# Kernel tuning notes

Measured on AMD Instinct MI355X. Metric: run time of the kernel, lower is better.

The kernel has to match this reference:

```python
import jax, jax.numpy as jnp
import numpy as np

B, N, DIM, NL, E = 8, 4096, 128, 3, 524288
NN = B * N


def setup_inputs() -> dict:
    key = jax.random.key(0)
    kx, ke, kw = jax.random.split(key, 3)
    x = jax.random.normal(kx, (B, N, DIM), dtype=jnp.float32)
    batch_edge_index = jax.random.randint(ke, (2, E), 0, NN, dtype=jnp.int32)
    wks = jax.random.split(kw, NL)
    Ws = jnp.stack([jax.random.normal(k, (DIM, DIM), dtype=jnp.float32) / np.sqrt(DIM)
                    for k in wks])  # [NL, DIM, DIM]
    bs = jnp.zeros((NL, DIM), dtype=jnp.float32)
    return {"x": x, "batch_edge_index": batch_edge_index, "Ws": Ws, "bs": bs}


def _gcn_layer(x, W, b, row, col, deg_inv_sqrt, n):
    # PyG GCNConv: h = x @ W; symmetric normalization over edges+self-loops;
    # scatter-add messages at targets (col); add bias.
    h = x @ W  # [n, DIM]
    norm = deg_inv_sqrt[row] * deg_inv_sqrt[col]  # [E+n]
    msg = h[row] * norm[:, None]  # gather at sources, scale
    return jax.ops.segment_sum(msg, col, num_segments=n) + b


def reference(x, batch_edge_index, Ws, bs):
    nb, npts, d = x.shape
    n = nb * npts
    h = x.reshape(n, d)
    # add self-loops once (same edge structure for all layers)
    loops = jnp.arange(n, dtype=batch_edge_index.dtype)
    row = jnp.concatenate([batch_edge_index[0], loops])
    col = jnp.concatenate([batch_edge_index[1], loops])
    deg = jax.ops.segment_sum(jnp.ones_like(col, dtype=h.dtype), col, num_segments=n)
    deg_inv_sqrt = jnp.where(deg > 0, jax.lax.rsqrt(jnp.maximum(deg, 1e-12)), 0.0)
    for i in range(NL):
        out = _gcn_layer(h, Ws[i], bs[i], row, col, deg_inv_sqrt, n)
        h = jax.nn.relu(h + out)  # residual + relu (dropout = identity in eval)
    return h.reshape(nb, npts, d)
```

## Files before the change

kernel.cpp:

```cpp
#include <hip/hip_runtime.h>


typedef __attribute__((ext_vector_type(8))) short short8;
typedef __attribute__((ext_vector_type(4))) float f32x4;
typedef __attribute__((ext_vector_type(2))) float f32x2;
typedef __attribute__((ext_vector_type(2))) unsigned u32x2;

__device__ inline ushort f2bf(float f) {
    union { float f; unsigned u; } v; v.f = f;
    unsigned u = v.u;
    return (ushort)((u + 0x7fffu + ((u >> 16) & 1u)) >> 16);
}
__device__ inline float2 bf2f(unsigned u) {
    union { unsigned i; float f; } a, b;
    a.i = u << 16;
    b.i = u & 0xffff0000u;
    return make_float2(a.f, b.f);
}
__device__ inline f32x4 bf4(u32x2 v) {
    float2 a = bf2f(v.x), b = bf2f(v.y);
    f32x4 r = { a.x, a.y, b.x, b.y };
    return r;
}
__device__ inline short8 pack8(f32x4 a, f32x4 b) {
    short8 r = { (short)f2bf(a.x), (short)f2bf(a.y), (short)f2bf(a.z), (short)f2bf(a.w),
                 (short)f2bf(b.x), (short)f2bf(b.y), (short)f2bf(b.z), (short)f2bf(b.w) };
    return r;
}
__device__ inline unsigned char f2fp8(float f) {
    return (unsigned char)(__builtin_amdgcn_cvt_pk_fp8_f32(f, f, 0, false) & 0xff);
}
__device__ inline f32x4 fp8x4(unsigned v) {
    f32x2 lo = __builtin_amdgcn_cvt_pk_f32_fp8((int)v, false);
    f32x2 hi = __builtin_amdgcn_cvt_pk_f32_fp8((int)v, true);
    f32x4 r = { lo.x, lo.y, hi.x, hi.y };
    return r;
}

__global__ void k_zero(int* __restrict__ p, int m) {
    int i = blockIdx.x * blockDim.x + threadIdx.x;
    if (i < m) p[i] = 0;
}

__global__ void k_deg(const int* __restrict__ col, int* __restrict__ deg, int E) {
    int i = blockIdx.x * blockDim.x + threadIdx.x;
    if (i < E) atomicAdd(&deg[col[i]], 1);
}

__global__ __launch_bounds__(256) void k_scan1(const int* __restrict__ deg,
                                               int* __restrict__ offs,
                                               int* __restrict__ bsum, int n) {
    __shared__ int sm[256];
    int t = threadIdx.x, i = blockIdx.x * 256 + t;
    int v = (i < n) ? deg[i] : 0;
    sm[t] = v;
    __syncthreads();
    for (int off = 1; off < 256; off <<= 1) {
        int u = (t >= off) ? sm[t - off] : 0;
        __syncthreads();
        sm[t] += u;
        __syncthreads();
    }
    if (i < n) offs[i] = sm[t] - v;
    if (t == 255) bsum[blockIdx.x] = sm[255];
}

__global__ __launch_bounds__(256) void k_scan3(int* __restrict__ offs,
                                               const int* __restrict__ bsum,
                                               const int* __restrict__ deg,
                                               int* __restrict__ cnt,
                                               float* __restrict__ dis,
                                               unsigned* __restrict__ g32,
                                               int n, int E) {
    __shared__ int red[256];
    int t = threadIdx.x, bid = blockIdx.x;
    red[t] = (t < 128 && t < bid) ? bsum[t] : 0;
    __syncthreads();
    for (int off = 128; off >= 1; off >>= 1) {
        if (t < off) red[t] += red[t + off];
        __syncthreads();
    }
    int base = red[0];
    int i = bid * 256 + t;
    if (i < n) {
        int o = offs[i] + base;
        offs[i] = o;
        cnt[i] = o;
        dis[i] = rsqrtf((float)(deg[i] + 1));
    }
    if (i == 0) offs[n] = E;
    if (i < 32) g32[(size_t)n * 32 + i] = 0;
}

#define GEMM_MAIN(A0, A1, A2, A3)                                               \
    f32x4 acc[8] = {};                                                          \
    _Pragma("unroll")                                                           \
    for (int nf = 0; nf < 8; ++nf) {                                            \
        const unsigned* wr = &Wl[nf * 16 + c][0];                               \
        int sx = (c & 7) << 2;                                                  \
        int b = q * 4;                                                          \
        short8 b0 = *(const short8*)(wr + ((b +  0) ^ sx));                     \
        short8 b1 = *(const short8*)(wr + ((b + 16) ^ sx));                     \
        short8 b2 = *(const short8*)(wr + ((b + 32) ^ sx));                     \
        short8 b3 = *(const short8*)(wr + ((b + 48) ^ sx));                     \
        acc[nf] = __builtin_amdgcn_mfma_f32_16x16x32_bf16(A0, b0, acc[nf], 0, 0, 0); \
        acc[nf] = __builtin_amdgcn_mfma_f32_16x16x32_bf16(A1, b1, acc[nf], 0, 0, 0); \
        acc[nf] = __builtin_amdgcn_mfma_f32_16x16x32_bf16(A2, b2, acc[nf], 0, 0, 0); \
        acc[nf] = __builtin_amdgcn_mfma_f32_16x16x32_bf16(A3, b3, acc[nf], 0, 0, 0); \
    }

#define GEMM_STORE(D0, D1, D2, D3)                                              \
    _Pragma("unroll")                                                           \
    for (int nf = 0; nf < 8; ++nf) {                                            \
        int gc = nf * 16 + c;                                                   \
        g[(size_t)(rb + q * 4 + 0) * 128 + gc] = f2fp8(acc[nf][0] * (D0));      \
        g[(size_t)(rb + q * 4 + 1) * 128 + gc] = f2fp8(acc[nf][1] * (D1));      \
        g[(size_t)(rb + q * 4 + 2) * 128 + gc] = f2fp8(acc[nf][2] * (D2));      \
        g[(size_t)(rb + q * 4 + 3) * 128 + gc] = f2fp8(acc[nf][3] * (D3));      \
    }

#define W_STAGE(TILE)                                                            \
    __shared__ unsigned Wl[128][64];                                             \
    int tid = threadIdx.x;                                                       \
    {                                                                            \
        int nn = tid & 127, hf = tid >> 7;                                       \
        for (int qq = 0; qq < 32; ++qq) {                                        \
            int k2 = hf * 32 + qq;                                               \
            float lo = W[(size_t)(2 * k2) * 128 + nn];                           \
            float hi = W[(size_t)(2 * k2 + 1) * 128 + nn];                       \
            Wl[nn][k2 ^ ((nn & 7) << 2)] = ((unsigned)f2bf(hi) << 16) | f2bf(lo);\
        }                                                                        \
    }                                                                            \
    __syncthreads();                                                             \
    int w = tid >> 6, l = tid & 63;                                              \
    int rb = (TILE) * 64 + w * 16;                                               \
    int c = l & 15, q = l >> 4;

__global__ __launch_bounds__(256) void k_gemm(const unsigned* __restrict__ hb,
                                              const float* __restrict__ W,
                                              const float* __restrict__ dis,
                                              unsigned char* __restrict__ g, int n) {
    W_STAGE(blockIdx.x)
    const short8* arow = (const short8*)(hb + (size_t)(rb + c) * 64);
    short8 a0 = __builtin_nontemporal_load(&arow[q]);
    short8 a1 = __builtin_nontemporal_load(&arow[4 + q]);
    short8 a2 = __builtin_nontemporal_load(&arow[8 + q]);
    short8 a3 = __builtin_nontemporal_load(&arow[12 + q]);
    GEMM_MAIN(a0, a1, a2, a3)
    float d0 = dis[rb + q * 4 + 0], d1 = dis[rb + q * 4 + 1];
    float d2 = dis[rb + q * 4 + 2], d3 = dis[rb + q * 4 + 3];
    GEMM_STORE(d0, d1, d2, d3)
}

__global__ __launch_bounds__(256) void k_l0b(const float* __restrict__ x,
                                             const float* __restrict__ W,
                                             const float* __restrict__ dis,
                                             unsigned char* __restrict__ g,
                                             const int* __restrict__ rowp,
                                             const int* __restrict__ colp,
                                             int* __restrict__ cnt,
                                             ushort* __restrict__ csru,
                                             int n, int E) {
    int gtiles = n >> 6;
    if ((int)blockIdx.x >= gtiles) {
        int i = ((int)blockIdx.x - gtiles) * 256 + threadIdx.x;
        if (i < E) {
            int cc = colp[i];
            int p = atomicAdd(&cnt[cc], 1);
            csru[p] = (ushort)rowp[i];
        }
        return;
    }
    W_STAGE((int)blockIdx.x)
    const f32x4* xr = (const f32x4*)(x + (size_t)(rb + c) * 128);
    short8 a0 = pack8(xr[q * 2 +  0], xr[q * 2 +  1]);
    short8 a1 = pack8(xr[q * 2 +  8], xr[q * 2 +  9]);
    short8 a2 = pack8(xr[q * 2 + 16], xr[q * 2 + 17]);
    short8 a3 = pack8(xr[q * 2 + 24], xr[q * 2 + 25]);
    GEMM_MAIN(a0, a1, a2, a3)
    float d0 = dis[rb + q * 4 + 0], d1 = dis[rb + q * 4 + 1];
    float d2 = dis[rb + q * 4 + 2], d3 = dis[rb + q * 4 + 3];
    GEMM_STORE(d0, d1, d2, d3)
}

__global__ __launch_bounds__(256) void k_gather(const unsigned* __restrict__ g32,
                                                unsigned* __restrict__ hb,
                                                const float* __restrict__ dis,
                                                const float* __restrict__ bias,
                                                const int* __restrict__ offs,
                                                const ushort* __restrict__ csru,
                                                const float* __restrict__ xres,
                                                float* __restrict__ outp,
                                                int n, int use_x, int last) {
    int wid = threadIdx.x >> 6, lane = threadIdx.x & 63;
    int sel = lane >> 5, hl = lane & 31;
    int node = blockIdx.x * 8 + wid * 2 + sel;
    if (node >= n) return;

    float dn = dis[node];
    f32x4 bv = ((const f32x4*)bias)[hl];
    f32x4 hv;
    if (use_x) {
        hv = __builtin_nontemporal_load(&((const f32x4*)xres)[(size_t)node * 32 + hl]);
    } else {
        u32x2 h2 = __builtin_nontemporal_load(&((const u32x2*)hb)[(size_t)node * 32 + hl]);
        hv = bf4(h2);
    }

    f32x4 acc = fp8x4(g32[(size_t)node * 32 + hl]);
    int s = offs[node];
    int deg = offs[node + 1] - s;
    for (int j0 = 0; j0 < deg; j0 += 32) {
        int rem = deg - j0;
        int m = rem < 32 ? rem : 32;
        int idx = (hl < m) ? (int)__builtin_nontemporal_load(&csru[s + j0 + hl]) : n;
        int mc = (m + 7) & ~7;
        unsigned v[32];
#pragma unroll
        for (int b = 0; b < 4; ++b) {
            if (b * 8 < mc) {
#pragma unroll
                for (int u = 0; u < 8; ++u) {
                    int r = __shfl(idx, b * 8 + u, 32);
                    v[b * 8 + u] = g32[(size_t)r * 32 + hl];
                }
            }
        }
#pragma unroll
        for (int b = 0; b < 4; ++b) {
            if (b * 8 < mc) {
                f32x4 s0 = (fp8x4(v[b * 8 + 0]) + fp8x4(v[b * 8 + 1])) +
                           (fp8x4(v[b * 8 + 2]) + fp8x4(v[b * 8 + 3]));
                f32x4 s1 = (fp8x4(v[b * 8 + 4]) + fp8x4(v[b * 8 + 5])) +
                           (fp8x4(v[b * 8 + 6]) + fp8x4(v[b * 8 + 7]));
                acc += s0 + s1;
            }
        }
    }

    f32x4 o = acc * dn + hv + bv;
    o.x = fmaxf(o.x, 0.f); o.y = fmaxf(o.y, 0.f);
    o.z = fmaxf(o.z, 0.f); o.w = fmaxf(o.w, 0.f);
    if (last) {
        __builtin_nontemporal_store(o, &((f32x4*)outp)[(size_t)node * 32 + hl]);
    } else {
        u32x2 pk;
        pk.x = ((unsigned)f2bf(o.y) << 16) | f2bf(o.x);
        pk.y = ((unsigned)f2bf(o.w) << 16) | f2bf(o.z);
        __builtin_nontemporal_store(pk, &((u32x2*)hb)[(size_t)node * 32 + hl]);
    }
}

static inline size_t al256(size_t x) { return (x + 255) & ~(size_t)255; }

extern "C" void kernel_launch(void* const* d_in, const int* in_sizes, int n_in,
                              void* d_out, int out_size, void* d_ws, size_t ws_size,
                              hipStream_t stream) {
    const float* x  = (const float*)d_in[0];
    const int*   ei = (const int*)d_in[1];
    const float* Ws = (const float*)d_in[2];
    const float* bs = (const float*)d_in[3];
    int n  = in_sizes[0] / 128;
    int E  = in_sizes[1] / 2;
    int NL = in_sizes[2] / (128 * 128);
    const int* rowp = ei;
    const int* colp = ei + E;

    char* ws = (char*)d_ws;
    size_t gplane  = al256((size_t)(n + 1) * 128);
    size_t hplane  = al256((size_t)(n + 1) * 256);
    unsigned char* g  = (unsigned char*)ws;
    unsigned*      hb = (unsigned*)(ws + gplane);
    char* p = ws + gplane + hplane;
    float* dis  = (float*)p;               p += al256((size_t)n * 4);
    int*   deg  = (int*)p;                 p += al256((size_t)n * 4);
    int*   offs = (int*)p;                 p += al256((size_t)(n + 1) * 4);
    int*   cnt  = (int*)p;                 p += al256((size_t)n * 4);
    int*   bsum = (int*)p;                 p += 512;
    ushort* csru = (ushort*)p;

    int nb = (n + 255) / 256;
    int gtiles = n / 64;
    int eblocks = (E + 255) / 256;

    k_zero<<<nb, 256, 0, stream>>>(deg, n);
    k_deg<<<eblocks, 256, 0, stream>>>(colp, deg, E);
    k_scan1<<<nb, 256, 0, stream>>>(deg, offs, bsum, n);
    k_scan3<<<nb, 256, 0, stream>>>(offs, bsum, deg, cnt, dis, (unsigned*)g, n, E);
    k_l0b<<<gtiles + eblocks, 256, 0, stream>>>(x, Ws, dis, g, rowp, colp,
                                                cnt, csru, n, E);

    for (int l = 0; l < NL; ++l) {
        int last = (l + 1 == NL);
        if (l > 0)
            k_gemm<<<gtiles, 256, 0, stream>>>(hb, Ws + (size_t)l * 128 * 128,
                                               dis, g, n);
        k_gather<<<(n + 7) / 8, 256, 0, stream>>>((const unsigned*)g, hb, dis,
                                                  bs + (size_t)l * 128,
                                                  offs, csru, x,
                                                  (float*)d_out, n,
                                                  l == 0, last);
    }
}
```

Measured before the change: 136.7 us.

## Fuse gather of layer l with next-layer GEMM via LDS, pre-transpose weights

Replaces the separate gather and GEMM kernels for intermediate layers with one kernel: each block aggregates 32 nodes, stores the bf16 result to LDS and global memory, then multiplies the tile by the next layer's weights with MFMA, writing fp8 messages into a second ping-pong buffer. Weights for later layers are converted to bf16 and transposed once by extra blocks in the setup kernel, so the fused kernel reads B fragments straight from global memory or cache instead of staging W into LDS per block. This removes one launch per layer and the re-read of h from global memory. In exchange each GEMM block has a small tile, every block re-reads the 32KB weight matrix from cache, and a second g buffer is added.

```diff
diff --git a/kernel.cpp b/kernel.cpp
--- a/kernel.cpp
+++ b/kernel.cpp
@@ -70,7 +70,8 @@
                                                const int* __restrict__ deg,
                                                int* __restrict__ cnt,
                                                float* __restrict__ dis,
-                                               unsigned* __restrict__ g32,
+                                               unsigned* __restrict__ ga32,
+                                               unsigned* __restrict__ gb32,
                                                int n, int E) {
     __shared__ int red[256];
     int t = threadIdx.x, bid = blockIdx.x;
@@ -89,35 +90,11 @@
         dis[i] = rsqrtf((float)(deg[i] + 1));
     }
     if (i == 0) offs[n] = E;
-    if (i < 32) g32[(size_t)n * 32 + i] = 0;
-}
-
-#define GEMM_MAIN(A0, A1, A2, A3)                                               \
-    f32x4 acc[8] = {};                                                          \
-    _Pragma("unroll")                                                           \
-    for (int nf = 0; nf < 8; ++nf) {                                            \
-        const unsigned* wr = &Wl[nf * 16 + c][0];                               \
-        int sx = (c & 7) << 2;                                                  \
-        int b = q * 4;                                                          \
-        short8 b0 = *(const short8*)(wr + ((b +  0) ^ sx));                     \
-        short8 b1 = *(const short8*)(wr + ((b + 16) ^ sx));                     \
-        short8 b2 = *(const short8*)(wr + ((b + 32) ^ sx));                     \
-        short8 b3 = *(const short8*)(wr + ((b + 48) ^ sx));                     \
-        acc[nf] = __builtin_amdgcn_mfma_f32_16x16x32_bf16(A0, b0, acc[nf], 0, 0, 0); \
-        acc[nf] = __builtin_amdgcn_mfma_f32_16x16x32_bf16(A1, b1, acc[nf], 0, 0, 0); \
-        acc[nf] = __builtin_amdgcn_mfma_f32_16x16x32_bf16(A2, b2, acc[nf], 0, 0, 0); \
-        acc[nf] = __builtin_amdgcn_mfma_f32_16x16x32_bf16(A3, b3, acc[nf], 0, 0, 0); \
-    }
-
-#define GEMM_STORE(D0, D1, D2, D3)                                              \
-    _Pragma("unroll")                                                           \
-    for (int nf = 0; nf < 8; ++nf) {                                            \
-        int gc = nf * 16 + c;                                                   \
-        g[(size_t)(rb + q * 4 + 0) * 128 + gc] = f2fp8(acc[nf][0] * (D0));      \
-        g[(size_t)(rb + q * 4 + 1) * 128 + gc] = f2fp8(acc[nf][1] * (D1));      \
-        g[(size_t)(rb + q * 4 + 2) * 128 + gc] = f2fp8(acc[nf][2] * (D2));      \
-        g[(size_t)(rb + q * 4 + 3) * 128 + gc] = f2fp8(acc[nf][3] * (D3));      \
-    }
+    if (i < 32) {
+        ga32[(size_t)n * 32 + i] = 0;
+        gb32[(size_t)n * 32 + i] = 0;
+    }
+}
 
 #define W_STAGE(TILE)                                                            \
     __shared__ unsigned Wl[128][64];                                             \
@@ -136,22 +113,6 @@
     int rb = (TILE) * 64 + w * 16;                                               \
     int c = l & 15, q = l >> 4;
 
-__global__ __launch_bounds__(256) void k_gemm(const unsigned* __restrict__ hb,
-                                              const float* __restrict__ W,
-                                              const float* __restrict__ dis,
-                                              unsigned char* __restrict__ g, int n) {
-    W_STAGE(blockIdx.x)
-    const short8* arow = (const short8*)(hb + (size_t)(rb + c) * 64);
-    short8 a0 = __builtin_nontemporal_load(&arow[q]);
-    short8 a1 = __builtin_nontemporal_load(&arow[4 + q]);
-    short8 a2 = __builtin_nontemporal_load(&arow[8 + q]);
-    short8 a3 = __builtin_nontemporal_load(&arow[12 + q]);
-    GEMM_MAIN(a0, a1, a2, a3)
-    float d0 = dis[rb + q * 4 + 0], d1 = dis[rb + q * 4 + 1];
-    float d2 = dis[rb + q * 4 + 2], d3 = dis[rb + q * 4 + 3];
-    GEMM_STORE(d0, d1, d2, d3)
-}
-
 __global__ __launch_bounds__(256) void k_l0b(const float* __restrict__ x,
                                              const float* __restrict__ W,
                                              const float* __restrict__ dis,
@@ -160,8 +121,24 @@
                                              const int* __restrict__ colp,
                                              int* __restrict__ cnt,
                                              ushort* __restrict__ csru,
-                                             int n, int E) {
+                                             unsigned* __restrict__ Wt,
+                                             int n, int E, int nwt) {
     int gtiles = n >> 6;
+    if ((int)blockIdx.x >= gtiles + ((E + 255) >> 8)) {
+        int wl = (int)blockIdx.x - gtiles - ((E + 255) >> 8);
+        if (wl < nwt) {
+            const float* Wsrc = W + (size_t)(wl + 1) * 128 * 128;
+            unsigned* Wd = Wt + (size_t)wl * 128 * 64;
+            int nn = threadIdx.x & 127, hf = threadIdx.x >> 7;
+            for (int qq = 0; qq < 32; ++qq) {
+                int k2 = hf * 32 + qq;
+                float lo = Wsrc[(size_t)(2 * k2) * 128 + nn];
+                float hi = Wsrc[(size_t)(2 * k2 + 1) * 128 + nn];
+                Wd[nn * 64 + k2] = ((unsigned)f2bf(hi) << 16) | f2bf(lo);
+            }
+        }
+        return;
+    }
     if ((int)blockIdx.x >= gtiles) {
         int i = ((int)blockIdx.x - gtiles) * 256 + threadIdx.x;
         if (i < E) {
@@ -177,36 +154,40 @@
     short8 a1 = pack8(xr[q * 2 +  8], xr[q * 2 +  9]);
     short8 a2 = pack8(xr[q * 2 + 16], xr[q * 2 + 17]);
     short8 a3 = pack8(xr[q * 2 + 24], xr[q * 2 + 25]);
-    GEMM_MAIN(a0, a1, a2, a3)
+    f32x4 acc[8] = {};
+#pragma unroll
+    for (int nf = 0; nf < 8; ++nf) {
+        const unsigned* wr = &Wl[nf * 16 + c][0];
+        int sx = (c & 7) << 2;
+        int b = q * 4;
+        short8 b0 = *(const short8*)(wr + ((b +  0) ^ sx));
+        short8 b1 = *(const short8*)(wr + ((b + 16) ^ sx));
+        short8 b2 = *(const short8*)(wr + ((b + 32) ^ sx));
+        short8 b3 = *(const short8*)(wr + ((b + 48) ^ sx));
+        acc[nf] = __builtin_amdgcn_mfma_f32_16x16x32_bf16(a0, b0, acc[nf], 0, 0, 0);
+        acc[nf] = __builtin_amdgcn_mfma_f32_16x16x32_bf16(a1, b1, acc[nf], 0, 0, 0);
+        acc[nf] = __builtin_amdgcn_mfma_f32_16x16x32_bf16(a2, b2, acc[nf], 0, 0, 0);
+        acc[nf] = __builtin_amdgcn_mfma_f32_16x16x32_bf16(a3, b3, acc[nf], 0, 0, 0);
+    }
     float d0 = dis[rb + q * 4 + 0], d1 = dis[rb + q * 4 + 1];
     float d2 = dis[rb + q * 4 + 2], d3 = dis[rb + q * 4 + 3];
-    GEMM_STORE(d0, d1, d2, d3)
-}
-
-__global__ __launch_bounds__(256) void k_gather(const unsigned* __restrict__ g32,
-                                                unsigned* __restrict__ hb,
-                                                const float* __restrict__ dis,
-                                                const float* __restrict__ bias,
-                                                const int* __restrict__ offs,
-                                                const ushort* __restrict__ csru,
-                                                const float* __restrict__ xres,
-                                                float* __restrict__ outp,
-                                                int n, int use_x, int last) {
-    int wid = threadIdx.x >> 6, lane = threadIdx.x & 63;
-    int sel = lane >> 5, hl = lane & 31;
-    int node = blockIdx.x * 8 + wid * 2 + sel;
-    if (node >= n) return;
-
+#pragma unroll
+    for (int nf = 0; nf < 8; ++nf) {
+        int gc = nf * 16 + c;
+        g[(size_t)(rb + q * 4 + 0) * 128 + gc] = f2fp8(acc[nf][0] * d0);
+        g[(size_t)(rb + q * 4 + 1) * 128 + gc] = f2fp8(acc[nf][1] * d1);
+        g[(size_t)(rb + q * 4 + 2) * 128 + gc] = f2fp8(acc[nf][2] * d2);
+        g[(size_t)(rb + q * 4 + 3) * 128 + gc] = f2fp8(acc[nf][3] * d3);
+    }
+}
+
+__device__ inline f32x4 gather_node(const unsigned* __restrict__ g32,
+                                    const float* __restrict__ dis,
+                                    const f32x4 bv, const f32x4 hv,
+                                    const int* __restrict__ offs,
+                                    const ushort* __restrict__ csru,
+                                    int node, int hl, int n) {
     float dn = dis[node];
-    f32x4 bv = ((const f32x4*)bias)[hl];
-    f32x4 hv;
-    if (use_x) {
-        hv = __builtin_nontemporal_load(&((const f32x4*)xres)[(size_t)node * 32 + hl]);
-    } else {
-        u32x2 h2 = __builtin_nontemporal_load(&((const u32x2*)hb)[(size_t)node * 32 + hl]);
-        hv = bf4(h2);
-    }
-
     f32x4 acc = fp8x4(g32[(size_t)node * 32 + hl]);
     int s = offs[node];
     int deg = offs[node + 1] - s;
@@ -237,18 +218,94 @@
             }
         }
     }
-
     f32x4 o = acc * dn + hv + bv;
     o.x = fmaxf(o.x, 0.f); o.y = fmaxf(o.y, 0.f);
     o.z = fmaxf(o.z, 0.f); o.w = fmaxf(o.w, 0.f);
-    if (last) {
-        __builtin_nontemporal_store(o, &((f32x4*)outp)[(size_t)node * 32 + hl]);
-    } else {
+    return o;
+}
+
+__global__ __launch_bounds__(256) void k_gq(const unsigned* __restrict__ gin,
+                                            unsigned char* __restrict__ gout,
+                                            unsigned* __restrict__ hb,
+                                            const float* __restrict__ dis,
+                                            const float* __restrict__ bias,
+                                            const int* __restrict__ offs,
+                                            const ushort* __restrict__ csru,
+                                            const float* __restrict__ xres,
+                                            const unsigned* __restrict__ Wt,
+                                            int n, int use_x) {
+    __shared__ unsigned Hs[32][68];
+    int tid = threadIdx.x;
+    int w = tid >> 6, lane = tid & 63;
+    int sel = lane >> 5, hl = lane & 31;
+
+    for (int it = 0; it < 4; ++it) {
+        int nl = w * 8 + it * 2 + sel;
+        int node = blockIdx.x * 32 + nl;
+        f32x4 bv = ((const f32x4*)bias)[hl];
+        f32x4 hv;
+        if (use_x) {
+            hv = __builtin_nontemporal_load(&((const f32x4*)xres)[(size_t)node * 32 + hl]);
+        } else {
+            u32x2 h2 = __builtin_nontemporal_load(&((const u32x2*)hb)[(size_t)node * 32 + hl]);
+            hv = bf4(h2);
+        }
+        f32x4 o = gather_node(gin, dis, bv, hv, offs, csru, node, hl, n);
         u32x2 pk;
         pk.x = ((unsigned)f2bf(o.y) << 16) | f2bf(o.x);
         pk.y = ((unsigned)f2bf(o.w) << 16) | f2bf(o.z);
         __builtin_nontemporal_store(pk, &((u32x2*)hb)[(size_t)node * 32 + hl]);
-    }
+        *(u32x2*)&Hs[nl][2 * hl] = pk;
+    }
+    __syncthreads();
+
+    int c = lane & 15, q = lane >> 4;
+    int r16 = (w & 1) * 16, ch2 = w >> 1;
+    const short8* ar = (const short8*)&Hs[r16 + c][0];
+    short8 a0 = *(const short8*)&Hs[r16 + c][q * 4 +  0];
+    short8 a1 = *(const short8*)&Hs[r16 + c][q * 4 + 16];
+    short8 a2 = *(const short8*)&Hs[r16 + c][q * 4 + 32];
+    short8 a3 = *(const short8*)&Hs[r16 + c][q * 4 + 48];
+    (void)ar;
+    f32x4 acc[4] = {};
+#pragma unroll
+    for (int nf = 0; nf < 4; ++nf) {
+        const short8* brow = (const short8*)(Wt + (size_t)(ch2 * 64 + nf * 16 + c) * 64);
+        short8 b0 = brow[q], b1 = brow[4 + q], b2 = brow[8 + q], b3 = brow[12 + q];
+        acc[nf] = __builtin_amdgcn_mfma_f32_16x16x32_bf16(a0, b0, acc[nf], 0, 0, 0);
+        acc[nf] = __builtin_amdgcn_mfma_f32_16x16x32_bf16(a1, b1, acc[nf], 0, 0, 0);
+        acc[nf] = __builtin_amdgcn_mfma_f32_16x16x32_bf16(a2, b2, acc[nf], 0, 0, 0);
+        acc[nf] = __builtin_amdgcn_mfma_f32_16x16x32_bf16(a3, b3, acc[nf], 0, 0, 0);
+    }
+    int grow = blockIdx.x * 32 + r16 + q * 4;
+    float d0 = dis[grow + 0], d1 = dis[grow + 1];
+    float d2 = dis[grow + 2], d3 = dis[grow + 3];
+#pragma unroll
+    for (int nf = 0; nf < 4; ++nf) {
+        int gc = ch2 * 64 + nf * 16 + c;
+        gout[(size_t)(grow + 0) * 128 + gc] = f2fp8(acc[nf][0] * d0);
+        gout[(size_t)(grow + 1) * 128 + gc] = f2fp8(acc[nf][1] * d1);
+        gout[(size_t)(grow + 2) * 128 + gc] = f2fp8(acc[nf][2] * d2);
+        gout[(size_t)(grow + 3) * 128 + gc] = f2fp8(acc[nf][3] * d3);
+    }
+}
+
+__global__ __launch_bounds__(256) void k_gather(const unsigned* __restrict__ g32,
+                                                const unsigned* __restrict__ hb,
+                                                const float* __restrict__ dis,
+                                                const float* __restrict__ bias,
+                                                const int* __restrict__ offs,
+                                                const ushort* __restrict__ csru,
+                                                float* __restrict__ outp, int n) {
+    int wid = threadIdx.x >> 6, lane = threadIdx.x & 63;
+    int sel = lane >> 5, hl = lane & 31;
+    int node = blockIdx.x * 8 + wid * 2 + sel;
+    if (node >= n) return;
+    f32x4 bv = ((const f32x4*)bias)[hl];
+    u32x2 h2 = __builtin_nontemporal_load(&((const u32x2*)hb)[(size_t)node * 32 + hl]);
+    f32x4 hv = bf4(h2);
+    f32x4 o = gather_node(g32, dis, bv, hv, offs, csru, node, hl, n);
+    __builtin_nontemporal_store(o, &((f32x4*)outp)[(size_t)node * 32 + hl]);
 }
 
 static inline size_t al256(size_t x) { return (x + 255) & ~(size_t)255; }
@@ -269,14 +326,16 @@
     char* ws = (char*)d_ws;
     size_t gplane  = al256((size_t)(n + 1) * 128);
     size_t hplane  = al256((size_t)(n + 1) * 256);
-    unsigned char* g  = (unsigned char*)ws;
-    unsigned*      hb = (unsigned*)(ws + gplane);
-    char* p = ws + gplane + hplane;
+    unsigned char* ga = (unsigned char*)ws;
+    unsigned char* gb = (unsigned char*)(ws + gplane);
+    unsigned*      hb = (unsigned*)(ws + 2 * gplane);
+    char* p = ws + 2 * gplane + hplane;
     float* dis  = (float*)p;               p += al256((size_t)n * 4);
     int*   deg  = (int*)p;                 p += al256((size_t)n * 4);
     int*   offs = (int*)p;                 p += al256((size_t)(n + 1) * 4);
     int*   cnt  = (int*)p;                 p += al256((size_t)n * 4);
     int*   bsum = (int*)p;                 p += 512;
+    unsigned* Wt = (unsigned*)p;           p += al256((size_t)(NL - 1) * 128 * 64 * 4);
     ushort* csru = (ushort*)p;
 
     int nb = (n + 255) / 256;
@@ -286,19 +345,20 @@
     k_zero<<<nb, 256, 0, stream>>>(deg, n);
     k_deg<<<eblocks, 256, 0, stream>>>(colp, deg, E);
     k_scan1<<<nb, 256, 0, stream>>>(deg, offs, bsum, n);
-    k_scan3<<<nb, 256, 0, stream>>>(offs, bsum, deg, cnt, dis, (unsigned*)g, n, E);
-    k_l0b<<<gtiles + eblocks, 256, 0, stream>>>(x, Ws, dis, g, rowp, colp,
-                                                cnt, csru, n, E);
-
-    for (int l = 0; l < NL; ++l) {
-        int last = (l + 1 == NL);
-        if (l > 0)
-            k_gemm<<<gtiles, 256, 0, stream>>>(hb, Ws + (size_t)l * 128 * 128,
-                                               dis, g, n);
-        k_gather<<<(n + 7) / 8, 256, 0, stream>>>((const unsigned*)g, hb, dis,
-                                                  bs + (size_t)l * 128,
-                                                  offs, csru, x,
-                                                  (float*)d_out, n,
-                                                  l == 0, last);
-    }
-}
+    k_scan3<<<nb, 256, 0, stream>>>(offs, bsum, deg, cnt, dis,
+                                    (unsigned*)ga, (unsigned*)gb, n, E);
+    k_l0b<<<gtiles + eblocks + (NL - 1), 256, 0, stream>>>(
+        x, Ws, dis, ga, rowp, colp, cnt, csru, Wt, n, E, NL - 1);
+
+    unsigned char* gcur = ga;
+    unsigned char* gnxt = gb;
+    for (int l = 0; l < NL - 1; ++l) {
+        k_gq<<<n / 32, 256, 0, stream>>>((const unsigned*)gcur, gnxt, hb, dis,
+                                         bs + (size_t)l * 128, offs, csru, x,
+                                         Wt + (size_t)l * 128 * 64, n, l == 0);
+        unsigned char* t = gcur; gcur = gnxt; gnxt = t;
+    }
+    k_gather<<<(n + 7) / 8, 256, 0, stream>>>((const unsigned*)gcur, hb, dis,
+                                              bs + (size_t)(NL - 1) * 128,
+                                              offs, csru, (float*)d_out, n);
+}
```

Result: no change. 135.4 us (-1.0%).
